# Performance work log

Hardware: AMD Instinct MI355X
Metric: run time of the kernel (lower is better)

## Reference

```python
import jax, jax.numpy as jnp
import numpy as np

EMB_DIM = 256
N_PTS = 2048  # decoder output points
LN_EPS = 1e-5


def setup_inputs() -> dict:
    key = jax.random.key(0)
    ks = jax.random.split(key, 20)
    B, N = 16, 4096

    def w(k, shape, fan_in):
        return (jax.random.normal(k, shape, dtype=jnp.float32) / np.sqrt(fan_in)).astype(jnp.float32)

    return {
        "in_pc": jax.random.normal(ks[0], (B, N, 3), dtype=jnp.float32),
        # encoder: 1x1 convs == per-point linear over channels
        "conv1_w": w(ks[1], (64, 3), 3),     "conv1_b": jnp.zeros((64,), jnp.float32),
        "conv2_w": w(ks[2], (128, 64), 64),  "conv2_b": jnp.zeros((128,), jnp.float32),
        "conv3_w": w(ks[3], (1024, 256), 256), "conv3_b": jnp.zeros((1024,), jnp.float32),
        "fc_enc_w": w(ks[4], (EMB_DIM, 1024), 1024), "fc_enc_b": jnp.zeros((EMB_DIM,), jnp.float32),
        # decoder
        "fc1_w": w(ks[5], (512, EMB_DIM), EMB_DIM), "fc1_b": jnp.zeros((512,), jnp.float32),
        "fc2_w": w(ks[6], (1024, 512), 512),        "fc2_b": jnp.zeros((1024,), jnp.float32),
        "fc3_w": w(ks[7], (3 * N_PTS, 1024), 1024), "fc3_b": jnp.zeros((3 * N_PTS,), jnp.float32),
        "ln_g": jnp.ones((3 * N_PTS,), jnp.float32), "ln_b": jnp.zeros((3 * N_PTS,), jnp.float32),
    }


def _pointwise(x, w, b):
    # x: (B, Cin, N), w: (Cout, Cin) -> (B, Cout, N)   (Conv1d with kernel=1)
    return jnp.einsum('bcn,oc->bon', x, w) + b[None, :, None]


def _chamfer(p, q):
    # p: (B,N,3), q: (B,M,3). Squared-L2 pairwise distance + min reductions.
    p2 = jnp.sum(p * p, axis=-1)                      # (B,N)
    q2 = jnp.sum(q * q, axis=-1)                      # (B,M)
    d = p2[:, :, None] + q2[:, None, :] - 2.0 * jnp.einsum('bnd,bmd->bnm', p, q)  # (B,N,M)
    return jnp.min(d, axis=2), jnp.min(d, axis=1)     # (B,N), (B,M)


def reference(in_pc, conv1_w, conv1_b, conv2_w, conv2_b, conv3_w, conv3_b,
              fc_enc_w, fc_enc_b, fc1_w, fc1_b, fc2_w, fc2_b, fc3_w, fc3_b,
              ln_g, ln_b):
    B, N, _ = in_pc.shape
    # ---- encoder ----
    xyz = jnp.transpose(in_pc, (0, 2, 1))            # (B,3,N)
    x = jax.nn.relu(_pointwise(xyz, conv1_w, conv1_b))   # (B,64,N)
    x = jax.nn.relu(_pointwise(x, conv2_w, conv2_b))     # (B,128,N)
    gfeat = jnp.max(x, axis=2, keepdims=True)            # (B,128,1) adaptive_max_pool1d(x,1)
    x0 = jnp.concatenate([x, jnp.broadcast_to(gfeat, (B, 128, N))], axis=1)  # (B,256,N)
    x = jax.nn.relu(_pointwise(x0, conv3_w, conv3_b))    # (B,1024,N)
    x = jnp.max(x, axis=2)                               # (B,1024)
    emb = x @ fc_enc_w.T + fc_enc_b                      # (B,EMB_DIM)
    # ---- decoder ----
    h = jax.nn.relu(emb @ fc1_w.T + fc1_b)               # (B,512)
    h = jax.nn.relu(h @ fc2_w.T + fc2_b)                 # (B,1024)
    h = h @ fc3_w.T + fc3_b                              # (B,3*N_PTS)
    mu = jnp.mean(h, axis=-1, keepdims=True)
    var = jnp.mean((h - mu) ** 2, axis=-1, keepdims=True)
    h = (h - mu) * jax.lax.rsqrt(var + LN_EPS) * ln_g + ln_b
    out_pc = h.reshape(B, -1, 3)                         # (B,N_PTS,3)
    # ---- chamfer reconstruction loss ----
    d1, d2 = _chamfer(in_pc, out_pc)
    loss = jnp.mean(d1) + jnp.mean(d2)
    return (x0, emb, out_pc, loss)
```

## Files before the change

kernel.cpp:

```cpp
#include <hip/hip_runtime.h>

#define OUT_X0   0
#define OUT_EMB  16777216
#define OUT_OPC  16781312
#define OUT_LOSS 16879616

#define OFF_GFEAT 0
#define OFF_POOL  8192
#define OFF_GCON  73728
#define OFF_EMB   139264
#define OFF_HD1   155648
#define OFF_HD2   188416
#define OFF_H3    253952
#define OFF_OPC   647168
#define OFF_D1M   1040384
#define OFF_D2M   1302528
#define OFF_PS    1433600
#define OFF_W3BF  1433984
#define H2_BYTES  (16u*1024*1024)

typedef short short8 __attribute__((ext_vector_type(8)));
typedef float f32x4  __attribute__((ext_vector_type(4)));

__device__ __forceinline__ unsigned short f2bf(float f){
  unsigned u = __float_as_uint(f);
  return (unsigned short)((u + 0x7FFFu + ((u >> 16) & 1u)) >> 16);
}

__global__ __launch_bounds__(256) void conv12_mfma(
    const float* __restrict__ in_pc,
    const float* __restrict__ w1, const float* __restrict__ b1,
    const float* __restrict__ w2, const float* __restrict__ b2,
    float* __restrict__ x0, unsigned short* __restrict__ h2b,
    unsigned* __restrict__ gfeatU,
    const float* __restrict__ w3, unsigned* __restrict__ w3bf)
{
  __shared__ unsigned short w2s[8192];
  __shared__ unsigned short h1s[8192];
  __shared__ float b2s[128];
  __shared__ unsigned gmax[128];
  int tid = threadIdx.x, bid = blockIdx.x;
  if (bid >= 512){
    int i = (bid-512)*256 + tid;
    float2 v = ((const float2*)w3)[i];
    w3bf[i] = (unsigned)f2bf(v.x) | ((unsigned)f2bf(v.y)<<16);
    return;
  }
  int b = bid >> 5;
  int nt0 = (bid & 31)*128;
  for (int i = tid; i < 2048; i += 256){
    int ch = i >> 4, q = i & 15;
    float4 v = ((const float4*)w2)[i];
    unsigned lo = (unsigned)f2bf(v.x) | ((unsigned)f2bf(v.y)<<16);
    unsigned hi = (unsigned)f2bf(v.z) | ((unsigned)f2bf(v.w)<<16);
    int byte = (ch*128 + q*8) ^ ((ch&7)<<4);
    *(uint2*)((char*)w2s + byte) = make_uint2(lo, hi);
  }
  if (tid < 128){ b2s[tid] = b2[tid]; gmax[tid] = 0u; }
  if (tid < 128){
    int idx = b*4096 + nt0 + tid;
    const float* p = in_pc + (size_t)idx*3;
    float px=p[0], py=p[1], pz=p[2];
    unsigned hp[32];
    #pragma unroll
    for (int q=0;q<32;q++){
      int c = q*2;
      float v0 = fmaxf(fmaf(w1[c*3  ],px, fmaf(w1[c*3+1],py, fmaf(w1[c*3+2],pz, b1[c  ]))), 0.f);
      float v1 = fmaxf(fmaf(w1[c*3+3],px, fmaf(w1[c*3+4],py, fmaf(w1[c*3+5],pz, b1[c+1]))), 0.f);
      hp[q] = (unsigned)f2bf(v0) | ((unsigned)f2bf(v1)<<16);
    }
    #pragma unroll
    for (int q=0;q<8;q++){
      int byte = (tid*128 + q*16) ^ ((tid&7)<<4);
      *(uint4*)((char*)h1s + byte) = make_uint4(hp[q*4],hp[q*4+1],hp[q*4+2],hp[q*4+3]);
    }
  }
  __syncthreads();
  int lane = tid & 63, w = tid >> 6;
  int g = lane >> 4, p15 = lane & 15;
  f32x4 acc[8][2] = {};
  #pragma unroll
  for (int ks=0; ks<2; ks++){
    int kb = (ks*32 + g*8)*2;
    short8 bfr[2];
    #pragma unroll
    for (int nf=0;nf<2;nf++){
      int pt = w*32 + nf*16 + p15;
      bfr[nf] = *(const short8*)((const char*)h1s + ((pt*128 + kb) ^ ((pt&7)<<4)));
    }
    #pragma unroll
    for (int mf=0;mf<8;mf++){
      int ch = mf*16 + p15;
      short8 af = *(const short8*)((const char*)w2s + ((ch*128 + kb) ^ ((ch&7)<<4)));
      acc[mf][0] = __builtin_amdgcn_mfma_f32_16x16x32_bf16(af, bfr[0], acc[mf][0], 0,0,0);
      acc[mf][1] = __builtin_amdgcn_mfma_f32_16x16x32_bf16(af, bfr[1], acc[mf][1], 0,0,0);
    }
  }
  int n_base = nt0 + w*32;
  #pragma unroll
  for (int mf=0; mf<8; mf++){
    int ch0 = mf*16 + g*4;
    float bias[4];
    #pragma unroll
    for (int j=0;j<4;j++) bias[j] = b2s[ch0+j];
    float vm[4] = {0.f,0.f,0.f,0.f};
    #pragma unroll
    for (int nf=0; nf<2; nf++){
      int n = n_base + nf*16 + p15;
      float v[4];
      #pragma unroll
      for (int j=0;j<4;j++){
        v[j] = fmaxf(acc[mf][nf][j] + bias[j], 0.f);
        vm[j] = fmaxf(vm[j], v[j]);
        x0[((size_t)(b*256 + ch0 + j))*4096 + n] = v[j];
      }
      unsigned lo = (unsigned)f2bf(v[0]) | ((unsigned)f2bf(v[1])<<16);
      unsigned hi = (unsigned)f2bf(v[2]) | ((unsigned)f2bf(v[3])<<16);
      *(uint2*)&h2b[((size_t)(b*4096 + n))*128 + ch0] = make_uint2(lo, hi);
    }
    #pragma unroll
    for (int j=0;j<4;j++){
      float m = vm[j];
      m = fmaxf(m, __shfl_xor(m,1));
      m = fmaxf(m, __shfl_xor(m,2));
      m = fmaxf(m, __shfl_xor(m,4));
      m = fmaxf(m, __shfl_xor(m,8));
      if (p15==0) atomicMax(&gmax[ch0+j], __float_as_uint(m));
    }
  }
  __syncthreads();
  if (tid < 128) atomicMax(&gfeatU[b*128 + tid], gmax[tid]);
}

__global__ __launch_bounds__(256) void bcast_gcon(
    const unsigned* __restrict__ gfeatU, float* __restrict__ x0,
    const float* __restrict__ w3, const float* __restrict__ b3,
    float* __restrict__ gcon)
{
  __shared__ float gf[2048];
  int tid = threadIdx.x;
  if (blockIdx.x < 8192){
    unsigned U = blockIdx.x*256 + tid;
    int n4 = U & 1023, c = (U >> 10) & 127, b = U >> 17;
    float g = __uint_as_float(gfeatU[b*128+c]);
    float4 v = {g,g,g,g};
    ((float4*)x0)[(((size_t)b*256 + 128 + c)*4096)/4 + n4] = v;
  } else {
    for (int i=tid;i<2048;i+=256) gf[i] = __uint_as_float(gfeatU[i]);
    __syncthreads();
    int o = (blockIdx.x - 8192)*256 + tid;
    float bias = b3[o];
    float acc[16];
    #pragma unroll
    for (int b=0;b<16;b++) acc[b]=bias;
    for (int c=0;c<128;c++){
      float wv = w3[(size_t)o*256 + 128 + c];
      #pragma unroll
      for (int b=0;b<16;b++) acc[b] += gf[b*128+c]*wv;
    }
    #pragma unroll
    for (int b=0;b<16;b++) gcon[b*1024+o] = acc[b];
  }
}

__global__ __launch_bounds__(512) void conv3_pool(
    const unsigned short* __restrict__ h2b, const unsigned short* __restrict__ w3b,
    const float* __restrict__ gcon, unsigned* __restrict__ pooled)
{
  __shared__ unsigned short Al[256*128];
  __shared__ unsigned short Bl[256*128];
  int mt = blockIdx.x, b = blockIdx.y;
  int tid = threadIdx.x;
  {
    const uint4* src = (const uint4*)(h2b + ((size_t)b*4096 + mt*256)*128);
    #pragma unroll
    for (int i=0;i<8;i++){
      int idx = i*512 + tid;
      int r = idx>>4, kc = idx&15;
      uint4 v = src[(size_t)r*16 + kc];
      int byte = (r*256 + kc*16) ^ ((r&7)<<4);
      *(uint4*)((char*)Al + byte) = v;
    }
  }
  int lane = tid & 63, wid = tid >> 6;
  int wm = wid >> 2, wn = wid & 3;
  int mbase = wm*128, nbase = wn*64;
  for (int nt=0; nt<4; nt++){
    if (nt) __syncthreads();
    {
      #pragma unroll
      for (int i=0;i<8;i++){
        int idx = i*512 + tid;
        int c = idx>>4, kc = idx&15;
        uint4 v = *(const uint4*)(w3b + ((size_t)(nt*256+c)*256 + kc*8));
        int byte = (c*256 + kc*16) ^ ((c&7)<<4);
        *(uint4*)((char*)Bl + byte) = v;
      }
    }
    __syncthreads();
    f32x4 acc[8][4] = {};
    #pragma unroll
    for (int ks=0;ks<4;ks++){
      int kb = (ks*32 + (lane>>4)*8)*2;
      short8 af[8], bfr[4];
      #pragma unroll
      for (int mi=0;mi<8;mi++){
        int row = mbase + mi*16 + (lane&15);
        af[mi] = *(const short8*)((const char*)Al + ((row*256 + kb) ^ ((row&7)<<4)));
      }
      #pragma unroll
      for (int ni=0;ni<4;ni++){
        int col = nbase + ni*16 + (lane&15);
        bfr[ni] = *(const short8*)((const char*)Bl + ((col*256 + kb) ^ ((col&7)<<4)));
      }
      #pragma unroll
      for (int mi=0;mi<8;mi++){
        #pragma unroll
        for (int ni=0;ni<4;ni++)
          acc[mi][ni] = __builtin_amdgcn_mfma_f32_16x16x32_bf16(af[mi], bfr[ni], acc[mi][ni], 0,0,0);
      }
    }
    #pragma unroll
    for (int ni=0;ni<4;ni++){
      int o = nt*256 + nbase + ni*16 + (lane&15);
      float g = gcon[b*1024 + o];
      float m = 0.f;
      #pragma unroll
      for (int mi=0;mi<8;mi++){
        f32x4 a = acc[mi][ni];
        #pragma unroll
        for (int r=0;r<4;r++){ float v = a[r]+g; m = fmaxf(m, v); }
      }
      m = fmaxf(m, 0.f);
      m = fmaxf(m, __shfl_xor(m, 16));
      m = fmaxf(m, __shfl_xor(m, 32));
      if (lane < 16) atomicMax(&pooled[(size_t)b*1024+o], __float_as_uint(m));
    }
  }
}

__global__ __launch_bounds__(256) void conv12_f32(
    const float* __restrict__ in_pc,
    const float* __restrict__ w1, const float* __restrict__ b1,
    const float* __restrict__ w2, const float* __restrict__ b2,
    float* __restrict__ x0, unsigned* __restrict__ gfeatU)
{
  __shared__ unsigned gmax[32];
  int tid = threadIdx.x;
  if (tid < 32) gmax[tid] = 0u;
  __syncthreads();
  int idx = blockIdx.x*256 + tid;
  int b = idx >> 12, n = idx & 4095;
  int gy = blockIdx.y;
  int lane = tid & 63;
  const float* p = in_pc + (size_t)idx*3;
  float px=p[0], py=p[1], pz=p[2];
  float h1[64];
  #pragma unroll
  for (int c=0;c<64;c++)
    h1[c] = fmaxf(w1[c*3]*px + w1[c*3+1]*py + w1[c*3+2]*pz + b1[c], 0.f);
  #pragma unroll
  for (int j=0;j<32;j++){
    int o = gy*32 + j;
    float a = b2[o];
    #pragma unroll
    for (int c=0;c<64;c++) a += w2[o*64+c]*h1[c];
    a = fmaxf(a, 0.f);
    x0[((size_t)b*256 + o)*4096 + n] = a;
    float m = a;
    #pragma unroll
    for (int off=32; off; off>>=1) m = fmaxf(m, __shfl_xor(m, off));
    if (lane==0) atomicMax(&gmax[j], __float_as_uint(m));
  }
  __syncthreads();
  if (tid < 32) atomicMax(&gfeatU[b*128 + gy*32 + tid], gmax[tid]);
}

__global__ __launch_bounds__(256) void conv3n(
    const float* __restrict__ x0, const unsigned* __restrict__ gfeatU,
    const float* __restrict__ w3, const float* __restrict__ b3,
    unsigned* __restrict__ pooled)
{
  __shared__ float wrow[8][256];
  int b = blockIdx.x >> 7, og = (blockIdx.x & 127)*8, tid = threadIdx.x;
  for (int i=tid;i<2048;i+=256){ int j=i>>8, c=i&255; wrow[j][c]=w3[(size_t)(og+j)*256+c]; }
  __syncthreads();
  float gconst[8];
  #pragma unroll
  for (int j=0;j<8;j++){
    float g = b3[og+j];
    for (int c=0;c<128;c++) g += __uint_as_float(gfeatU[b*128+c])*wrow[j][128+c];
    gconst[j] = g;
  }
  const float* xb = x0 + (size_t)b*256*4096;
  float m[8];
  #pragma unroll
  for (int j=0;j<8;j++) m[j]=0.f;
  for (int n=tid;n<4096;n+=256){
    float v[8];
    #pragma unroll
    for (int j=0;j<8;j++) v[j]=gconst[j];
    for (int c=0;c<128;c++){
      float xv = xb[(size_t)c*4096 + n];
      #pragma unroll
      for (int j=0;j<8;j++) v[j] += xv*wrow[j][c];
    }
    #pragma unroll
    for (int j=0;j<8;j++) m[j] = fmaxf(m[j], v[j]);
  }
  #pragma unroll
  for (int j=0;j<8;j++){
    float v = m[j];
    for (int off=32; off; off>>=1) v = fmaxf(v, __shfl_xor(v, off));
    if ((tid&63)==0) atomicMax(&pooled[(size_t)b*1024+og+j], __float_as_uint(v));
  }
}

template<bool RELU>
__global__ __launch_bounds__(256) void fc_wave16(
    const float* __restrict__ A, const float* __restrict__ W,
    const float* __restrict__ bias, float* __restrict__ out,
    float* __restrict__ out2, int K, int O)
{
  int lane = threadIdx.x & 63, w = threadIdx.x >> 6;
  int o = blockIdx.x*4 + w;
  const float* Wr = W + (size_t)o*K;
  float acc[16];
  #pragma unroll
  for (int b=0;b<16;b++) acc[b]=0.f;
  for (int k = lane*4; k < K; k += 256){
    float4 wv = *(const float4*)&Wr[k];
    #pragma unroll
    for (int b=0;b<16;b++){
      float4 av = *(const float4*)&A[(size_t)b*K + k];
      acc[b] += wv.x*av.x + wv.y*av.y + wv.z*av.z + wv.w*av.w;
    }
  }
  #pragma unroll
  for (int b=0;b<16;b++){
    float v = acc[b];
    #pragma unroll
    for (int off=32; off; off>>=1) v += __shfl_xor(v, off);
    if (lane==0){
      v += bias[o];
      if (RELU) v = fmaxf(v, 0.f);
      out[(size_t)b*O+o] = v;
      if (out2) out2[(size_t)b*O+o] = v;
    }
  }
}

__global__ __launch_bounds__(256) void lnorm(
    const float* __restrict__ h3, const float* __restrict__ g,
    const float* __restrict__ be, float* __restrict__ outf,
    float* __restrict__ outb)
{
  int b = blockIdx.x, tid = threadIdx.x;
  const float* x = h3 + b*6144;
  float s=0.f, s2=0.f;
  for (int i=tid;i<6144;i+=256){ float v=x[i]; s+=v; s2+=v*v; }
  for (int off=32; off; off>>=1){ s += __shfl_xor(s,off); s2 += __shfl_xor(s2,off); }
  __shared__ float red[8];
  int lane = tid&63, wid = tid>>6;
  if (lane==0){ red[wid]=s; red[4+wid]=s2; }
  __syncthreads();
  s  = red[0]+red[1]+red[2]+red[3];
  s2 = red[4]+red[5]+red[6]+red[7];
  float mu  = s * (1.f/6144.f);
  float var = s2 * (1.f/6144.f) - mu*mu;
  float inv = rsqrtf(var + 1e-5f);
  for (int i=tid;i<6144;i+=256){
    float v = (x[i]-mu)*inv*g[i] + be[i];
    outf[b*6144+i] = v;
    outb[b*6144+i] = v;
  }
}

__global__ __launch_bounds__(256) void chamfer_all(
    const float* __restrict__ in_pc, const float* __restrict__ opc,
    unsigned* __restrict__ d1m, unsigned* __restrict__ d2m)
{
  __shared__ float sx[256], sy[256], sz[256], s2[256];
  int bid = blockIdx.x, tid = threadIdx.x;
  const float* stage;
  const float* qry;
  unsigned* outp;
  if (bid < 2048){
    int xt = bid & 15, b = (bid >> 4) & 15, mt = bid >> 8;
    stage = opc + b*6144 + mt*768;
    qry   = in_pc + ((size_t)b*4096 + xt*256 + tid)*3;
    outp  = d1m + b*4096 + xt*256 + tid;
  } else {
    int r = bid - 2048;
    int xt = r & 7, b = (r >> 3) & 15, nt = r >> 7;
    stage = in_pc + ((size_t)b*4096 + nt*256)*3;
    qry   = opc + b*6144 + (xt*256 + tid)*3;
    outp  = d2m + b*2048 + xt*256 + tid;
  }
  {
    const float* S = stage + tid*3;
    float x=S[0], y=S[1], z=S[2];
    sx[tid]=x; sy[tid]=y; sz[tid]=z; s2[tid]=x*x+y*y+z*z;
  }
  __syncthreads();
  float qx=qry[0], qy=qry[1], qz=qry[2];
  float p2 = qx*qx + qy*qy + qz*qz;
  float ma=3.0e38f, mb=3.0e38f;
  #pragma unroll 2
  for (int i=0;i<64;i++){
    float4 X  = *(const float4*)&sx[i*4];
    float4 Y  = *(const float4*)&sy[i*4];
    float4 Z  = *(const float4*)&sz[i*4];
    float4 Q2 = *(const float4*)&s2[i*4];
    float t;
    t = fmaf(-2.f, fmaf(qx,X.x,fmaf(qy,Y.x,qz*Z.x)), Q2.x); ma = fminf(ma,t);
    t = fmaf(-2.f, fmaf(qx,X.y,fmaf(qy,Y.y,qz*Z.y)), Q2.y); mb = fminf(mb,t);
    t = fmaf(-2.f, fmaf(qx,X.z,fmaf(qy,Y.z,qz*Z.z)), Q2.z); ma = fminf(ma,t);
    t = fmaf(-2.f, fmaf(qx,X.w,fmaf(qy,Y.w,qz*Z.w)), Q2.w); mb = fminf(mb,t);
  }
  float d = fmaxf(p2 + fminf(ma, mb), 0.f);
  atomicMin(outp, __float_as_uint(d));
}

__global__ __launch_bounds__(256) void sum_part(
    const unsigned* __restrict__ d1m, const unsigned* __restrict__ d2m,
    float* __restrict__ ps)
{
  int bid = blockIdx.x, tid = threadIdx.x;
  const unsigned* src = (bid<64) ? (d1m + bid*1024) : (d2m + (size_t)(bid-64)*1024);
  float s = 0.f;
  for (int i=tid;i<1024;i+=256) s += __uint_as_float(src[i]);
  for (int off=32; off; off>>=1) s += __shfl_xor(s,off);
  __shared__ float red[4];
  if ((tid&63)==0) red[tid>>6]=s;
  __syncthreads();
  if (tid==0) ps[bid] = red[0]+red[1]+red[2]+red[3];
}

__global__ void loss_k(const float* __restrict__ ps, float* __restrict__ out){
  int tid = threadIdx.x;
  float v = 0.f;
  if (tid < 64) v = ps[tid] * (1.0f/65536.0f);
  else if (tid < 96) v = ps[tid] * (1.0f/32768.0f);
  for (int off=32; off; off>>=1) v += __shfl_xor(v,off);
  __shared__ float red[2];
  if ((tid&63)==0) red[tid>>6]=v;
  __syncthreads();
  if (tid==0) out[0] = red[0]+red[1];
}

extern "C" void kernel_launch(void* const* d_in, const int* in_sizes, int n_in,
                              void* d_out, int out_size, void* d_ws, size_t ws_size,
                              hipStream_t stream)
{
  (void)in_sizes; (void)n_in; (void)out_size;
  const float* in_pc = (const float*)d_in[0];
  const float* w1   = (const float*)d_in[1];
  const float* b1   = (const float*)d_in[2];
  const float* w2   = (const float*)d_in[3];
  const float* b2   = (const float*)d_in[4];
  const float* w3   = (const float*)d_in[5];
  const float* b3   = (const float*)d_in[6];
  const float* wenc = (const float*)d_in[7];
  const float* benc = (const float*)d_in[8];
  const float* wf1  = (const float*)d_in[9];
  const float* bfc1 = (const float*)d_in[10];
  const float* wf2  = (const float*)d_in[11];
  const float* bfc2 = (const float*)d_in[12];
  const float* wf3  = (const float*)d_in[13];
  const float* bfc3 = (const float*)d_in[14];
  const float* lng  = (const float*)d_in[15];
  const float* lnb  = (const float*)d_in[16];
  float* out = (float*)d_out;

  bool big = ws_size >= (size_t)(H2_BYTES + 2*1024*1024);
  char* ws = (char*)d_ws;
  unsigned short* h2b = (unsigned short*)ws;
  char* small = ws + (big ? H2_BYTES : 0);

  unsigned* gfeatU = (unsigned*)(small + OFF_GFEAT);
  float* pooled = (float*)(small + OFF_POOL);
  float* gcon = (float*)(small + OFF_GCON);
  float* emb  = (float*)(small + OFF_EMB);
  float* hd1  = (float*)(small + OFF_HD1);
  float* hd2  = (float*)(small + OFF_HD2);
  float* h3   = (float*)(small + OFF_H3);
  float* opc  = (float*)(small + OFF_OPC);
  unsigned* d1m = (unsigned*)(small + OFF_D1M);
  unsigned* d2m = (unsigned*)(small + OFF_D2M);
  float* ps   = (float*)(small + OFF_PS);
  unsigned short* w3b = (unsigned short*)(small + OFF_W3BF);

  hipMemsetAsync(small + OFF_GFEAT, 0, 8192 + 65536, stream);
  hipMemsetAsync(small + OFF_D1M, 0x7F, 262144 + 131072, stream);

  if (big){
    conv12_mfma<<<1024, 256, 0, stream>>>(in_pc, w1, b1, w2, b2, out, h2b, gfeatU,
                                          w3, (unsigned*)w3b);
    bcast_gcon<<<8196, 256, 0, stream>>>(gfeatU, out, w3, b3, gcon);
    conv3_pool<<<dim3(16,16), 512, 0, stream>>>(h2b, w3b, gcon, (unsigned*)pooled);
  } else {
    conv12_f32<<<dim3(256,4), 256, 0, stream>>>(in_pc, w1, b1, w2, b2, out, gfeatU);
    bcast_gcon<<<8196, 256, 0, stream>>>(gfeatU, out, w3, b3, gcon);
    conv3n<<<2048, 256, 0, stream>>>(out, gfeatU, w3, b3, (unsigned*)pooled);
  }
  fc_wave16<false><<<64,   256, 0, stream>>>(pooled, wenc, benc, emb, out + OUT_EMB, 1024, 256);
  fc_wave16<true ><<<128,  256, 0, stream>>>(emb, wf1, bfc1, hd1, nullptr, 256, 512);
  fc_wave16<true ><<<256,  256, 0, stream>>>(hd1, wf2, bfc2, hd2, nullptr, 512, 1024);
  fc_wave16<false><<<1536, 256, 0, stream>>>(hd2, wf3, bfc3, h3, nullptr, 1024, 6144);
  lnorm<<<16, 256, 0, stream>>>(h3, lng, lnb, opc, out + OUT_OPC);
  chamfer_all<<<4096, 256, 0, stream>>>(in_pc, opc, d1m, d2m);
  sum_part<<<96, 256, 0, stream>>>(d1m, d2m, ps);
  loss_k<<<1, 128, 0, stream>>>(ps, out + OUT_LOSS);
}
```

Before: 167.0 us.

## Shrink conv3 tiles, parallelize conv1 across all threads, fuse loss kernels, tweak chamfer

conv3_pool switches to 128x128 tiles with a doubled grid, giving more blocks and smaller LDS use so occupancy rises, at the cost of reloading the w3 tiles more often. conv12_mfma now has all 256 threads compute conv1, each producing half the channels of a point, where before only 128 did. The chamfer loop prescales the staged coordinates by -2 and keeps four running minima for more instruction-level parallelism. sum_part and loss_k are merged into one kernel that uses a last-block atomic counter, reset inside lnorm, which removes one launch.

```diff
diff --git a/kernel.cpp b/kernel.cpp
--- a/kernel.cpp
+++ b/kernel.cpp
@@ -17,6 +17,7 @@
 #define OFF_D2M   1302528
 #define OFF_PS    1433600
 #define OFF_W3BF  1433984
+#define OFF_CNT   1958272
 #define H2_BYTES  (16u*1024*1024)
 
 typedef short short8 __attribute__((ext_vector_type(8)));
@@ -57,22 +58,24 @@
     *(uint2*)((char*)w2s + byte) = make_uint2(lo, hi);
   }
   if (tid < 128){ b2s[tid] = b2[tid]; gmax[tid] = 0u; }
-  if (tid < 128){
-    int idx = b*4096 + nt0 + tid;
+  {
+    int pt = tid & 127;
+    int qb = (tid >> 7) * 16;
+    int idx = b*4096 + nt0 + pt;
     const float* p = in_pc + (size_t)idx*3;
     float px=p[0], py=p[1], pz=p[2];
-    unsigned hp[32];
-    #pragma unroll
-    for (int q=0;q<32;q++){
-      int c = q*2;
+    unsigned hp[16];
+    #pragma unroll
+    for (int q=0;q<16;q++){
+      int c = (qb + q)*2;
       float v0 = fmaxf(fmaf(w1[c*3  ],px, fmaf(w1[c*3+1],py, fmaf(w1[c*3+2],pz, b1[c  ]))), 0.f);
       float v1 = fmaxf(fmaf(w1[c*3+3],px, fmaf(w1[c*3+4],py, fmaf(w1[c*3+5],pz, b1[c+1]))), 0.f);
       hp[q] = (unsigned)f2bf(v0) | ((unsigned)f2bf(v1)<<16);
     }
     #pragma unroll
-    for (int q=0;q<8;q++){
-      int byte = (tid*128 + q*16) ^ ((tid&7)<<4);
-      *(uint4*)((char*)h1s + byte) = make_uint4(hp[q*4],hp[q*4+1],hp[q*4+2],hp[q*4+3]);
+    for (int t=0;t<4;t++){
+      int byte = (pt*128 + qb*4 + t*16) ^ ((pt&7)<<4);
+      *(uint4*)((char*)h1s + byte) = make_uint4(hp[t*4],hp[t*4+1],hp[t*4+2],hp[t*4+3]);
     }
   }
   __syncthreads();
@@ -167,66 +170,66 @@
     const unsigned short* __restrict__ h2b, const unsigned short* __restrict__ w3b,
     const float* __restrict__ gcon, unsigned* __restrict__ pooled)
 {
-  __shared__ unsigned short Al[256*128];
-  __shared__ unsigned short Bl[256*128];
+  __shared__ unsigned short Al[128*128];
+  __shared__ unsigned short Bl[128*128];
   int mt = blockIdx.x, b = blockIdx.y;
   int tid = threadIdx.x;
   {
-    const uint4* src = (const uint4*)(h2b + ((size_t)b*4096 + mt*256)*128);
-    #pragma unroll
-    for (int i=0;i<8;i++){
+    const uint4* src = (const uint4*)(h2b + ((size_t)b*4096 + mt*128)*128);
+    #pragma unroll
+    for (int i=0;i<4;i++){
       int idx = i*512 + tid;
       int r = idx>>4, kc = idx&15;
-      uint4 v = src[(size_t)r*16 + kc];
+      uint4 v = src[idx];
       int byte = (r*256 + kc*16) ^ ((r&7)<<4);
       *(uint4*)((char*)Al + byte) = v;
     }
   }
   int lane = tid & 63, wid = tid >> 6;
   int wm = wid >> 2, wn = wid & 3;
-  int mbase = wm*128, nbase = wn*64;
-  for (int nt=0; nt<4; nt++){
+  int mbase = wm*64, nbase = wn*32;
+  for (int nt=0; nt<8; nt++){
     if (nt) __syncthreads();
     {
       #pragma unroll
-      for (int i=0;i<8;i++){
+      for (int i=0;i<4;i++){
         int idx = i*512 + tid;
         int c = idx>>4, kc = idx&15;
-        uint4 v = *(const uint4*)(w3b + ((size_t)(nt*256+c)*256 + kc*8));
+        uint4 v = *(const uint4*)(w3b + ((size_t)(nt*128+c)*256 + kc*8));
         int byte = (c*256 + kc*16) ^ ((c&7)<<4);
         *(uint4*)((char*)Bl + byte) = v;
       }
     }
     __syncthreads();
-    f32x4 acc[8][4] = {};
+    f32x4 acc[4][2] = {};
     #pragma unroll
     for (int ks=0;ks<4;ks++){
       int kb = (ks*32 + (lane>>4)*8)*2;
-      short8 af[8], bfr[4];
-      #pragma unroll
-      for (int mi=0;mi<8;mi++){
+      short8 af[4], bfr[2];
+      #pragma unroll
+      for (int mi=0;mi<4;mi++){
         int row = mbase + mi*16 + (lane&15);
         af[mi] = *(const short8*)((const char*)Al + ((row*256 + kb) ^ ((row&7)<<4)));
       }
       #pragma unroll
-      for (int ni=0;ni<4;ni++){
+      for (int ni=0;ni<2;ni++){
         int col = nbase + ni*16 + (lane&15);
         bfr[ni] = *(const short8*)((const char*)Bl + ((col*256 + kb) ^ ((col&7)<<4)));
       }
       #pragma unroll
-      for (int mi=0;mi<8;mi++){
+      for (int mi=0;mi<4;mi++){
         #pragma unroll
-        for (int ni=0;ni<4;ni++)
+        for (int ni=0;ni<2;ni++)
           acc[mi][ni] = __builtin_amdgcn_mfma_f32_16x16x32_bf16(af[mi], bfr[ni], acc[mi][ni], 0,0,0);
       }
     }
     #pragma unroll
-    for (int ni=0;ni<4;ni++){
-      int o = nt*256 + nbase + ni*16 + (lane&15);
+    for (int ni=0;ni<2;ni++){
+      int o = nt*128 + nbase + ni*16 + (lane&15);
       float g = gcon[b*1024 + o];
       float m = 0.f;
       #pragma unroll
-      for (int mi=0;mi<8;mi++){
+      for (int mi=0;mi<4;mi++){
         f32x4 a = acc[mi][ni];
         #pragma unroll
         for (int r=0;r<4;r++){ float v = a[r]+g; m = fmaxf(m, v); }
@@ -353,9 +356,10 @@
 __global__ __launch_bounds__(256) void lnorm(
     const float* __restrict__ h3, const float* __restrict__ g,
     const float* __restrict__ be, float* __restrict__ outf,
-    float* __restrict__ outb)
+    float* __restrict__ outb, int* __restrict__ cnt)
 {
   int b = blockIdx.x, tid = threadIdx.x;
+  if (b==0 && tid==0) *cnt = 0;
   const float* x = h3 + b*6144;
   float s=0.f, s2=0.f;
   for (int i=tid;i<6144;i+=256){ float v=x[i]; s+=v; s2+=v*v; }
@@ -380,7 +384,7 @@
     const float* __restrict__ in_pc, const float* __restrict__ opc,
     unsigned* __restrict__ d1m, unsigned* __restrict__ d2m)
 {
-  __shared__ float sx[256], sy[256], sz[256], s2[256];
+  __shared__ float sX[256], sY[256], sZ[256], sQ[256];
   int bid = blockIdx.x, tid = threadIdx.x;
   const float* stage;
   const float* qry;
@@ -400,53 +404,59 @@
   {
     const float* S = stage + tid*3;
     float x=S[0], y=S[1], z=S[2];
-    sx[tid]=x; sy[tid]=y; sz[tid]=z; s2[tid]=x*x+y*y+z*z;
+    sX[tid]=-2.f*x; sY[tid]=-2.f*y; sZ[tid]=-2.f*z; sQ[tid]=x*x+y*y+z*z;
   }
   __syncthreads();
   float qx=qry[0], qy=qry[1], qz=qry[2];
   float p2 = qx*qx + qy*qy + qz*qz;
-  float ma=3.0e38f, mb=3.0e38f;
-  #pragma unroll 2
+  float ma=3.0e38f, mb=3.0e38f, mc=3.0e38f, md=3.0e38f;
+  #pragma unroll 4
   for (int i=0;i<64;i++){
-    float4 X  = *(const float4*)&sx[i*4];
-    float4 Y  = *(const float4*)&sy[i*4];
-    float4 Z  = *(const float4*)&sz[i*4];
-    float4 Q2 = *(const float4*)&s2[i*4];
+    float4 X = *(const float4*)&sX[i*4];
+    float4 Y = *(const float4*)&sY[i*4];
+    float4 Z = *(const float4*)&sZ[i*4];
+    float4 Q = *(const float4*)&sQ[i*4];
     float t;
-    t = fmaf(-2.f, fmaf(qx,X.x,fmaf(qy,Y.x,qz*Z.x)), Q2.x); ma = fminf(ma,t);
-    t = fmaf(-2.f, fmaf(qx,X.y,fmaf(qy,Y.y,qz*Z.y)), Q2.y); mb = fminf(mb,t);
-    t = fmaf(-2.f, fmaf(qx,X.z,fmaf(qy,Y.z,qz*Z.z)), Q2.z); ma = fminf(ma,t);
-    t = fmaf(-2.f, fmaf(qx,X.w,fmaf(qy,Y.w,qz*Z.w)), Q2.w); mb = fminf(mb,t);
-  }
-  float d = fmaxf(p2 + fminf(ma, mb), 0.f);
+    t = fmaf(qx,X.x, fmaf(qy,Y.x, fmaf(qz,Z.x, Q.x))); ma = fminf(ma,t);
+    t = fmaf(qx,X.y, fmaf(qy,Y.y, fmaf(qz,Z.y, Q.y))); mb = fminf(mb,t);
+    t = fmaf(qx,X.z, fmaf(qy,Y.z, fmaf(qz,Z.z, Q.z))); mc = fminf(mc,t);
+    t = fmaf(qx,X.w, fmaf(qy,Y.w, fmaf(qz,Z.w, Q.w))); md = fminf(md,t);
+  }
+  float d = fmaxf(p2 + fminf(fminf(ma,mb), fminf(mc,md)), 0.f);
   atomicMin(outp, __float_as_uint(d));
 }
 
-__global__ __launch_bounds__(256) void sum_part(
+__global__ __launch_bounds__(256) void sum_loss(
     const unsigned* __restrict__ d1m, const unsigned* __restrict__ d2m,
-    float* __restrict__ ps)
+    float* __restrict__ ps, int* __restrict__ cnt, float* __restrict__ out)
 {
   int bid = blockIdx.x, tid = threadIdx.x;
-  const unsigned* src = (bid<64) ? (d1m + bid*1024) : (d2m + (size_t)(bid-64)*1024);
-  float s = 0.f;
-  for (int i=tid;i<1024;i+=256) s += __uint_as_float(src[i]);
-  for (int off=32; off; off>>=1) s += __shfl_xor(s,off);
   __shared__ float red[4];
-  if ((tid&63)==0) red[tid>>6]=s;
-  __syncthreads();
-  if (tid==0) ps[bid] = red[0]+red[1]+red[2]+red[3];
-}
-
-__global__ void loss_k(const float* __restrict__ ps, float* __restrict__ out){
-  int tid = threadIdx.x;
+  __shared__ int last;
+  {
+    const unsigned* src = (bid<64) ? (d1m + bid*1024) : (d2m + (size_t)(bid-64)*1024);
+    float s = 0.f;
+    for (int i=tid;i<1024;i+=256) s += __uint_as_float(src[i]);
+    for (int off=32; off; off>>=1) s += __shfl_xor(s,off);
+    if ((tid&63)==0) red[tid>>6]=s;
+    __syncthreads();
+    if (tid==0){
+      ps[bid] = red[0]+red[1]+red[2]+red[3];
+      __threadfence();
+      last = (atomicAdd(cnt, 1) == 95);
+    }
+    __syncthreads();
+  }
+  if (!last) return;
+  __threadfence();
   float v = 0.f;
   if (tid < 64) v = ps[tid] * (1.0f/65536.0f);
   else if (tid < 96) v = ps[tid] * (1.0f/32768.0f);
   for (int off=32; off; off>>=1) v += __shfl_xor(v,off);
-  __shared__ float red[2];
+  __syncthreads();
   if ((tid&63)==0) red[tid>>6]=v;
   __syncthreads();
-  if (tid==0) out[0] = red[0]+red[1];
+  if (tid==0) out[0] = red[0]+red[1]+red[2]+red[3];
 }
 
 extern "C" void kernel_launch(void* const* d_in, const int* in_sizes, int n_in,
@@ -490,6 +500,7 @@
   unsigned* d2m = (unsigned*)(small + OFF_D2M);
   float* ps   = (float*)(small + OFF_PS);
   unsigned short* w3b = (unsigned short*)(small + OFF_W3BF);
+  int* cnt = (int*)(small + OFF_CNT);
 
   hipMemsetAsync(small + OFF_GFEAT, 0, 8192 + 65536, stream);
   hipMemsetAsync(small + OFF_D1M, 0x7F, 262144 + 131072, stream);
@@ -498,7 +509,7 @@
     conv12_mfma<<<1024, 256, 0, stream>>>(in_pc, w1, b1, w2, b2, out, h2b, gfeatU,
                                           w3, (unsigned*)w3b);
     bcast_gcon<<<8196, 256, 0, stream>>>(gfeatU, out, w3, b3, gcon);
-    conv3_pool<<<dim3(16,16), 512, 0, stream>>>(h2b, w3b, gcon, (unsigned*)pooled);
+    conv3_pool<<<dim3(32,16), 512, 0, stream>>>(h2b, w3b, gcon, (unsigned*)pooled);
   } else {
     conv12_f32<<<dim3(256,4), 256, 0, stream>>>(in_pc, w1, b1, w2, b2, out, gfeatU);
     bcast_gcon<<<8196, 256, 0, stream>>>(gfeatU, out, w3, b3, gcon);
@@ -508,8 +519,7 @@
   fc_wave16<true ><<<128,  256, 0, stream>>>(emb, wf1, bfc1, hd1, nullptr, 256, 512);
   fc_wave16<true ><<<256,  256, 0, stream>>>(hd1, wf2, bfc2, hd2, nullptr, 512, 1024);
   fc_wave16<false><<<1536, 256, 0, stream>>>(hd2, wf3, bfc3, h3, nullptr, 1024, 6144);
-  lnorm<<<16, 256, 0, stream>>>(h3, lng, lnb, opc, out + OUT_OPC);
+  lnorm<<<16, 256, 0, stream>>>(h3, lng, lnb, opc, out + OUT_OPC, cnt);
   chamfer_all<<<4096, 256, 0, stream>>>(in_pc, opc, d1m, d2m);
-  sum_part<<<96, 256, 0, stream>>>(d1m, d2m, ps);
-  loss_k<<<1, 128, 0, stream>>>(ps, out + OUT_LOSS);
-}
+  sum_loss<<<96, 256, 0, stream>>>(d1m, d2m, ps, cnt, out + OUT_LOSS);
+}
```

After: 166.1 us. No clear change (-0.5%).
